# Optimization experiments

Measured on AMD Instinct MI355X. Metric: run time of the kernel, lower is better.

The kernel has to match this reference:

```python
import jax, jax.numpy as jnp
import numpy as np


def _pairwise_sqdist(a, b):
    # a: [B,N,2], b: [B,M,2] -> [B,N,M] squared Euclidean distances
    a2 = jnp.sum(a * a, axis=-1)  # [B,N]
    b2 = jnp.sum(b * b, axis=-1)  # [B,M]
    ab = jnp.einsum('bnd,bmd->bnm', a, b)  # [B,N,M]
    return a2[:, :, None] + b2[:, None, :] - 2.0 * ab


def setup_inputs() -> dict:
    key = jax.random.key(0)
    k1, k2 = jax.random.split(key)
    B, N, M, D = 16, 2048, 2048, 2
    preds = jax.random.normal(k1, (B, N, D), dtype=jnp.float32)
    targs = jax.random.normal(k2, (B, M, D), dtype=jnp.float32)
    subcoef = jnp.ones((D,), dtype=jnp.float32)
    return {"preds": preds, "targs": targs, "subcoef": subcoef}


def reference(preds, targs, subcoef):
    # Bidirectional Chamfer-style NN L1 loss, faithful to NNLoss.nn_loss.
    d2 = _pairwise_sqdist(preds, targs)  # [B,N,M]

    # preds -> nearest GT (KDTree over targs queried with preds)
    nn_t = jnp.argmin(d2, axis=2)  # [B,N]
    matched_t = jnp.take_along_axis(targs, nn_t[:, :, None], axis=1)  # [B,N,2]
    move_preds_to_gt = jnp.sum(jnp.abs(preds - matched_t) * subcoef)

    # targs -> nearest pred (KDTree over preds queried with targs)
    nn_p = jnp.argmin(d2, axis=1)  # [B,M]
    matched_p = jnp.take_along_axis(preds, nn_p[:, :, None], axis=1)  # [B,M,2]
    move_gts_to_pred = jnp.sum(jnp.abs(matched_p - targs))

    return move_gts_to_pred + move_preds_to_gt
```

## Files before the change

### kernel.cpp

```cpp
#include <hip/hip_runtime.h>


typedef float v2f __attribute__((ext_vector_type(2)));

constexpr int   NPTS = 2048;
constexpr int   NB   = 128;
constexpr float XMIN = -5.0f;
constexpr float BW   = 0.078125f;
constexpr float INVW = 12.8f;
constexpr float SLCK = 1e-5f;

constexpr size_t RECS_OFF  = 0;
constexpr size_t START_OFF = 32 * NPTS * 16;

__device__ __forceinline__ int xbucket(float x) {
    int bk = (int)((x - XMIN) * INVW);
    return bk < 0 ? 0 : (bk > NB - 1 ? NB - 1 : bk);
}

__device__ __forceinline__ unsigned long long shflx64(unsigned long long v, int m) {
    unsigned int lo = (unsigned int)v, hi = (unsigned int)(v >> 32);
    lo = __shfl_xor(lo, m, 64);
    hi = __shfl_xor(hi, m, 64);
    return ((unsigned long long)hi << 32) | lo;
}

__global__ __launch_bounds__(1024) void build_sorted(
    const float* __restrict__ preds, const float* __restrict__ targs,
    float4* __restrict__ recs, int* __restrict__ gstart)
{
    __shared__ int cnt[NB];
    __shared__ int ofs[NB];
    __shared__ int wtot;

    const int s   = blockIdx.x;
    const int t   = s >> 4;
    const int b   = s & 15;
    const int tid = threadIdx.x;
    const float* src = (t == 0 ? preds : targs) + b * (NPTS * 2);

    if (tid < NB) cnt[tid] = 0;
    __syncthreads();

    const float4 f = reinterpret_cast<const float4*>(src)[tid];
    const int bk0 = xbucket(f.x);
    const int bk1 = xbucket(f.z);
    atomicAdd(&cnt[bk0], 1);
    atomicAdd(&cnt[bk1], 1);
    __syncthreads();

    const int lane = tid & 63;
    int v = (tid < NB) ? cnt[tid] : 0;
    #pragma unroll
    for (int off = 1; off < 64; off <<= 1) {
        const int u = __shfl_up(v, off, 64);
        if (lane >= off) v += u;
    }
    if (tid == 63) wtot = v;
    __syncthreads();
    if (tid >= 64 && tid < NB) v += wtot;
    if (tid < NB) {
        const int ex = v - cnt[tid];
        ofs[tid] = ex;
        gstart[s * (NB + 1) + tid] = ex;
    }
    if (tid == 0) gstart[s * (NB + 1) + NB] = NPTS;
    __syncthreads();

    {
        const int p0 = atomicAdd(&ofs[bk0], 1);
        recs[s * NPTS + p0] = {f.x, f.y, __int_as_float(2 * tid), 0.0f};
        const int p1 = atomicAdd(&ofs[bk1], 1);
        recs[s * NPTS + p1] = {f.z, f.w, __int_as_float(2 * tid + 1), 0.0f};
    }
}

__global__ __launch_bounds__(256) void nn_pruned(
    const float* __restrict__ preds, const float* __restrict__ targs,
    const float* __restrict__ subcoef, float* __restrict__ out,
    const float4* __restrict__ recs, const int* __restrict__ gstart)
{
    __shared__ float4 pl[NPTS];
    __shared__ int    st[NB + 1];
    __shared__ float  ssum[4];

    const int blk = blockIdx.x;
    const int tid = threadIdx.x;
    const int dir  = blk >> 9;
    const int b    = (blk >> 5) & 15;
    const int tile = blk & 31;

    const int qset = (dir ? 16 : 0) + b;
    const int dset = (dir ? 0 : 16) + b;

    {
        const float4* P = recs + dset * NPTS;
        #pragma unroll
        for (int k = 0; k < NPTS / 256; ++k)
            pl[tid + k * 256] = P[tid + k * 256];
        if (tid <= NB) st[tid] = gstart[dset * (NB + 1) + tid];
    }

    const int qs  = tile * 64 + (tid >> 2);
    const int sub = tid & 3;
    const float4 qr = recs[qset * NPTS + qs];
    const float qx = qr.x, qy = qr.y;

    float xmn = qx, xmx = qx;
    #pragma unroll
    for (int m = 1; m < 64; m <<= 1) {
        xmn = fminf(xmn, __shfl_xor(xmn, m, 64));
        xmx = fmaxf(xmx, __shfl_xor(xmx, m, 64));
    }
    __syncthreads();

    int blo = xbucket(xmn) - 1; blo = blo < 0 ? 0 : blo;
    int bhi = xbucket(xmx) + 1; bhi = bhi > NB - 1 ? NB - 1 : bhi;

    unsigned long long best = 0x7F800000FFFFFFFFull;

    int jlo = st[blo];
    int jhi = st[bhi + 1];

    #define SCAN(a, bnd)                                                        \
        for (int j = (a) + sub; j < (bnd); j += 4) {                            \
            const float4 r = pl[j];                                             \
            const float dx = qx - r.x, dy = qy - r.y;                           \
            const float d2 = fmaf(dx, dx, dy * dy);                             \
            const unsigned long long pk =                                       \
                ((unsigned long long)__float_as_uint(d2) << 32) |               \
                (unsigned int)__float_as_int(r.z);                              \
            best = pk < best ? pk : best;                                       \
        }

    SCAN(jlo, jhi)

    while (true) {
        unsigned long long o = shflx64(best, 1); best = o < best ? o : best;
        o = shflx64(best, 2);                    best = o < best ? o : best;
        const float bd = __uint_as_float((unsigned int)(best >> 32));
        const float lb = fmaxf(qx - fmaf((float)blo, BW, XMIN) - SLCK, 0.0f);
        const float rb = fmaxf(fmaf((float)(bhi + 1), BW, XMIN) - qx - SLCK, 0.0f);
        const bool nl = (blo > 0)      && (lb * lb <= bd);
        const bool nr = (bhi < NB - 1) && (rb * rb <= bd);
        const bool aL = __any(nl), aR = __any(nr);
        if (!aL && !aR) break;
        if (aL) { --blo; const int a = st[blo];      SCAN(a, jlo)   jlo = a; }
        if (aR) { ++bhi; const int e = st[bhi + 1];  SCAN(jhi, e)   jhi = e; }
    }
    #undef SCAN

    float val = 0.0f;
    if (sub == 0) {
        const int idx = (int)(unsigned int)best;
        const float2* dbo = reinterpret_cast<const float2*>(dir ? preds : targs)
                            + b * NPTS;
        const float2 tp = dbo[idx];
        float sx = 1.0f, sy = 1.0f;
        if (dir == 0) { sx = subcoef[0]; sy = subcoef[1]; }
        val = fabsf(qx - tp.x) * sx + fabsf(qy - tp.y) * sy;
    }

    #pragma unroll
    for (int off = 32; off > 0; off >>= 1)
        val += __shfl_down(val, off, 64);
    if ((tid & 63) == 0) ssum[tid >> 6] = val;
    __syncthreads();
    if (tid == 0) {
        const float s2 = ssum[0] + ssum[1] + ssum[2] + ssum[3];
        atomicAdd(out, s2);
    }
}

extern "C" void kernel_launch(void* const* d_in, const int* in_sizes, int n_in,
                              void* d_out, int out_size, void* d_ws, size_t ws_size,
                              hipStream_t stream) {
    const float* preds   = (const float*)d_in[0];
    const float* targs   = (const float*)d_in[1];
    const float* subcoef = (const float*)d_in[2];
    float* out = (float*)d_out;

    float4* recs = (float4*)((char*)d_ws + RECS_OFF);
    int*    gst  = (int*)((char*)d_ws + START_OFF);

    build_sorted<<<32, 1024, 0, stream>>>(preds, targs, recs, gst);
    nn_pruned<<<1024, 256, 0, stream>>>(preds, targs, subcoef, out, recs, gst);
}
```

Measured before the change: 88.76 us.

## Fuse bucket sort into NN search kernel, per-query unsorted processing

Merges the two kernels into one. Each block now bucket-sorts the whole database set into LDS itself instead of reading pre-sorted records from a workspace, which removes one launch and the global round trip. Queries are taken in original (unsorted) order with 128 queries per 512-thread block. The per-wavefront x-range window and the wave-wide __any ring expansion become per-lane decisions. The cost is that every block redoes the 2048-point sort (16 blocks per set). Because queries are unsorted, lanes in a wave search different buckets, so divergence rises.

```diff
diff --git a/kernel.cpp b/kernel.cpp
--- a/kernel.cpp
+++ b/kernel.cpp
@@ -1,7 +1,5 @@
 #include <hip/hip_runtime.h>
 
-
-typedef float v2f __attribute__((ext_vector_type(2)));
 
 constexpr int   NPTS = 2048;
 constexpr int   NB   = 128;
@@ -10,8 +8,10 @@
 constexpr float INVW = 12.8f;
 constexpr float SLCK = 1e-5f;
 
-constexpr size_t RECS_OFF  = 0;
-constexpr size_t START_OFF = 32 * NPTS * 16;
+constexpr int BLK   = 512;
+constexpr int QPB   = 128;
+constexpr int TILES = NPTS / QPB;
+constexpr int NBLK  = 2 * 16 * TILES;
 
 __device__ __forceinline__ int xbucket(float x) {
     int bk = (int)((x - XMIN) * INVW);
@@ -25,100 +25,82 @@
     return ((unsigned long long)hi << 32) | lo;
 }
 
-__global__ __launch_bounds__(1024) void build_sorted(
+__global__ __launch_bounds__(BLK) void nn_fused(
     const float* __restrict__ preds, const float* __restrict__ targs,
-    float4* __restrict__ recs, int* __restrict__ gstart)
+    const float* __restrict__ subcoef, float* __restrict__ out)
 {
-    __shared__ int cnt[NB];
-    __shared__ int ofs[NB];
-    __shared__ int wtot;
+    __shared__ float4 pl[NPTS];
+    __shared__ int    st[NB + 1];
+    __shared__ int    cnt[NB];
+    __shared__ int    ofs[NB];
+    __shared__ int    wtot_s;
+    __shared__ float  ssum[BLK / 64];
 
-    const int s   = blockIdx.x;
-    const int t   = s >> 4;
-    const int b   = s & 15;
+    const int blk = blockIdx.x;
     const int tid = threadIdx.x;
-    const float* src = (t == 0 ? preds : targs) + b * (NPTS * 2);
+    const int dir  = blk >> 8;
+    const int b    = (blk >> 4) & 15;
+    const int tile = blk & 15;
+
+    const float* qsrc = (dir == 0 ? preds : targs) + b * (NPTS * 2);
+    const float* dsrc = (dir == 0 ? targs : preds) + b * (NPTS * 2);
 
     if (tid < NB) cnt[tid] = 0;
+    const float4* d4 = reinterpret_cast<const float4*>(dsrc);
+    const float4 r0 = d4[tid];
+    const float4 r1 = d4[tid + BLK];
     __syncthreads();
 
-    const float4 f = reinterpret_cast<const float4*>(src)[tid];
-    const int bk0 = xbucket(f.x);
-    const int bk1 = xbucket(f.z);
-    atomicAdd(&cnt[bk0], 1);
-    atomicAdd(&cnt[bk1], 1);
-    __syncthreads();
-
-    const int lane = tid & 63;
-    int v = (tid < NB) ? cnt[tid] : 0;
-    #pragma unroll
-    for (int off = 1; off < 64; off <<= 1) {
-        const int u = __shfl_up(v, off, 64);
-        if (lane >= off) v += u;
-    }
-    if (tid == 63) wtot = v;
-    __syncthreads();
-    if (tid >= 64 && tid < NB) v += wtot;
-    if (tid < NB) {
-        const int ex = v - cnt[tid];
-        ofs[tid] = ex;
-        gstart[s * (NB + 1) + tid] = ex;
-    }
-    if (tid == 0) gstart[s * (NB + 1) + NB] = NPTS;
+    const int k0 = xbucket(r0.x), k1 = xbucket(r0.z);
+    const int k2 = xbucket(r1.x), k3 = xbucket(r1.z);
+    atomicAdd(&cnt[k0], 1);
+    atomicAdd(&cnt[k1], 1);
+    atomicAdd(&cnt[k2], 1);
+    atomicAdd(&cnt[k3], 1);
     __syncthreads();
 
     {
-        const int p0 = atomicAdd(&ofs[bk0], 1);
-        recs[s * NPTS + p0] = {f.x, f.y, __int_as_float(2 * tid), 0.0f};
-        const int p1 = atomicAdd(&ofs[bk1], 1);
-        recs[s * NPTS + p1] = {f.z, f.w, __int_as_float(2 * tid + 1), 0.0f};
-    }
-}
-
-__global__ __launch_bounds__(256) void nn_pruned(
-    const float* __restrict__ preds, const float* __restrict__ targs,
-    const float* __restrict__ subcoef, float* __restrict__ out,
-    const float4* __restrict__ recs, const int* __restrict__ gstart)
-{
-    __shared__ float4 pl[NPTS];
-    __shared__ int    st[NB + 1];
-    __shared__ float  ssum[4];
-
-    const int blk = blockIdx.x;
-    const int tid = threadIdx.x;
-    const int dir  = blk >> 9;
-    const int b    = (blk >> 5) & 15;
-    const int tile = blk & 31;
-
-    const int qset = (dir ? 16 : 0) + b;
-    const int dset = (dir ? 0 : 16) + b;
-
-    {
-        const float4* P = recs + dset * NPTS;
+        const int lane = tid & 63;
+        int v = (tid < NB) ? cnt[tid] : 0;
         #pragma unroll
-        for (int k = 0; k < NPTS / 256; ++k)
-            pl[tid + k * 256] = P[tid + k * 256];
-        if (tid <= NB) st[tid] = gstart[dset * (NB + 1) + tid];
-    }
-
-    const int qs  = tile * 64 + (tid >> 2);
-    const int sub = tid & 3;
-    const float4 qr = recs[qset * NPTS + qs];
-    const float qx = qr.x, qy = qr.y;
-
-    float xmn = qx, xmx = qx;
-    #pragma unroll
-    for (int m = 1; m < 64; m <<= 1) {
-        xmn = fminf(xmn, __shfl_xor(xmn, m, 64));
-        xmx = fmaxf(xmx, __shfl_xor(xmx, m, 64));
+        for (int off = 1; off < 64; off <<= 1) {
+            const int u = __shfl_up(v, off, 64);
+            if (lane >= off) v += u;
+        }
+        if (tid == 63) wtot_s = v;
+        __syncthreads();
+        if (tid >= 64 && tid < NB) v += wtot_s;
+        if (tid < NB) {
+            const int ex = v - cnt[tid];
+            ofs[tid] = ex;
+            st[tid]  = ex;
+        }
+        if (tid == 0) st[NB] = NPTS;
     }
     __syncthreads();
 
-    int blo = xbucket(xmn) - 1; blo = blo < 0 ? 0 : blo;
-    int bhi = xbucket(xmx) + 1; bhi = bhi > NB - 1 ? NB - 1 : bhi;
+    {
+        int p;
+        p = atomicAdd(&ofs[k0], 1);
+        pl[p] = {r0.x, r0.y, __int_as_float(2 * tid), 0.0f};
+        p = atomicAdd(&ofs[k1], 1);
+        pl[p] = {r0.z, r0.w, __int_as_float(2 * tid + 1), 0.0f};
+        p = atomicAdd(&ofs[k2], 1);
+        pl[p] = {r1.x, r1.y, __int_as_float(2 * (tid + BLK)), 0.0f};
+        p = atomicAdd(&ofs[k3], 1);
+        pl[p] = {r1.z, r1.w, __int_as_float(2 * (tid + BLK) + 1), 0.0f};
+    }
+    __syncthreads();
+
+    const int qi  = tile * QPB + (tid >> 2);
+    const int sub = tid & 3;
+    const float2 qp = reinterpret_cast<const float2*>(qsrc)[qi];
+    const float qx = qp.x, qy = qp.y;
+
+    int blo = xbucket(qx) - 1; blo = blo < 0 ? 0 : blo;
+    int bhi = xbucket(qx) + 1; bhi = bhi > NB - 1 ? NB - 1 : bhi;
 
     unsigned long long best = 0x7F800000FFFFFFFFull;
-
     int jlo = st[blo];
     int jhi = st[bhi + 1];
 
@@ -143,19 +125,16 @@
         const float rb = fmaxf(fmaf((float)(bhi + 1), BW, XMIN) - qx - SLCK, 0.0f);
         const bool nl = (blo > 0)      && (lb * lb <= bd);
         const bool nr = (bhi < NB - 1) && (rb * rb <= bd);
-        const bool aL = __any(nl), aR = __any(nr);
-        if (!aL && !aR) break;
-        if (aL) { --blo; const int a = st[blo];      SCAN(a, jlo)   jlo = a; }
-        if (aR) { ++bhi; const int e = st[bhi + 1];  SCAN(jhi, e)   jhi = e; }
+        if (!nl && !nr) break;
+        if (nl) { --blo; const int a = st[blo];      SCAN(a, jlo)   jlo = a; }
+        if (nr) { ++bhi; const int e = st[bhi + 1];  SCAN(jhi, e)   jhi = e; }
     }
     #undef SCAN
 
     float val = 0.0f;
     if (sub == 0) {
         const int idx = (int)(unsigned int)best;
-        const float2* dbo = reinterpret_cast<const float2*>(dir ? preds : targs)
-                            + b * NPTS;
-        const float2 tp = dbo[idx];
+        const float2 tp = reinterpret_cast<const float2*>(dsrc)[idx];
         float sx = 1.0f, sy = 1.0f;
         if (dir == 0) { sx = subcoef[0]; sy = subcoef[1]; }
         val = fabsf(qx - tp.x) * sx + fabsf(qy - tp.y) * sy;
@@ -167,8 +146,10 @@
     if ((tid & 63) == 0) ssum[tid >> 6] = val;
     __syncthreads();
     if (tid == 0) {
-        const float s2 = ssum[0] + ssum[1] + ssum[2] + ssum[3];
-        atomicAdd(out, s2);
+        float s = ssum[0];
+        #pragma unroll
+        for (int w = 1; w < BLK / 64; ++w) s += ssum[w];
+        atomicAdd(out, s);
     }
 }
 
@@ -180,9 +161,5 @@
     const float* subcoef = (const float*)d_in[2];
     float* out = (float*)d_out;
 
-    float4* recs = (float4*)((char*)d_ws + RECS_OFF);
-    int*    gst  = (int*)((char*)d_ws + START_OFF);
-
-    build_sorted<<<32, 1024, 0, stream>>>(preds, targs, recs, gst);
-    nn_pruned<<<1024, 256, 0, stream>>>(preds, targs, subcoef, out, recs, gst);
+    nn_fused<<<NBLK, BLK, 0, stream>>>(preds, targs, subcoef, out);
 }
```

After: 88.53 us. No clear change (-0.3%).
